# Kernel tuning notes

Measured on AMD Instinct MI355X. Metric: run time of the kernel, lower is better.

Reference implementation:

```python
import jax, jax.numpy as jnp
import numpy as np

N_NODES = 100000
N_EDGES = 1600000
D_IN, D_HID, D_OUT = 128, 128, 64


def _mean_agg(h_src_feat, src, dst, num_nodes):
    # gather source features along edges, scatter-sum into destinations,
    # divide by in-degree (clamped to 1, matching DGL zero-degree handling)
    summed = jax.ops.segment_sum(h_src_feat[src], dst, num_segments=num_nodes)
    deg = jax.ops.segment_sum(jnp.ones((src.shape[0],), h_src_feat.dtype), dst,
                              num_segments=num_nodes)
    return summed / jnp.maximum(deg, 1.0)[:, None]


def setup_inputs() -> dict:
    key = jax.random.key(0)
    ks = jax.random.split(key, 8)
    x = jax.random.normal(ks[0], (N_NODES, D_IN), dtype=jnp.float32)
    src = jax.random.randint(ks[1], (N_EDGES,), 0, N_NODES, dtype=jnp.int64)
    dst = jax.random.randint(ks[2], (N_EDGES,), 0, N_NODES, dtype=jnp.int64)
    s1 = 1.0 / np.sqrt(D_IN)
    s2 = 1.0 / np.sqrt(D_HID)
    W_self1 = jax.random.normal(ks[3], (D_IN, D_HID), dtype=jnp.float32) * s1
    W_neigh1 = jax.random.normal(ks[4], (D_IN, D_HID), dtype=jnp.float32) * s1
    b1 = jnp.zeros((D_HID,), dtype=jnp.float32)
    W_self2 = jax.random.normal(ks[5], (D_HID, D_OUT), dtype=jnp.float32) * s2
    W_neigh2 = jax.random.normal(ks[6], (D_HID, D_OUT), dtype=jnp.float32) * s2
    b2 = jnp.zeros((D_OUT,), dtype=jnp.float32)
    return {"x": x, "src": src, "dst": dst,
            "W_self1": W_self1, "W_neigh1": W_neigh1, "b1": b1,
            "W_self2": W_self2, "W_neigh2": W_neigh2, "b2": b2}


def reference(x, src, dst, W_self1, W_neigh1, b1, W_self2, W_neigh2, b2):
    n = x.shape[0]
    # layer 1: SAGEConv(mean) + ReLU (dropout is identity in eval mode)
    agg1 = _mean_agg(x, src, dst, n)
    h = x @ W_self1 + agg1 @ W_neigh1 + b1
    h = jax.nn.relu(h)
    # layer 2: SAGEConv(mean)
    agg2 = _mean_agg(h, src, dst, n)
    out = h @ W_self2 + agg2 @ W_neigh2 + b2
    return out
```

## Files before the change

kernel.cpp:

```cpp
#include <hip/hip_runtime.h>

#define N_NODES 100000
#define N_EDGES 1600000
#define D 128
#define D_OUT 64
#define MAXDEG 64

#define NBUCK 196
#define BCAP  12288
#define CHUNK 6400
#define NBLK_A (N_EDGES / CHUNK)
#define NBLK_CVT 6250
#define NBLK_PACK 24

typedef __attribute__((ext_vector_type(8))) short short8;
typedef __attribute__((ext_vector_type(4))) float floatx4;
typedef __attribute__((ext_vector_type(2))) float floatx2;

__device__ inline unsigned short f2bf(float f) {
    unsigned u = __builtin_bit_cast(unsigned, f);
    u = (u + 0x7fffu + ((u >> 16) & 1u)) >> 16;
    return (unsigned short)u;
}

__device__ inline void pack_dev(const float* __restrict__ Wa, const float* __restrict__ Wb,
                                int ncols, unsigned short* __restrict__ out, int t) {
    int nnt = ncols >> 4;
    int lane = t & 63;
    int nt = (t >> 6) % nnt;
    int kt = t / (64 * nnt);
    int col = nt * 16 + (lane & 15);
    int k0 = kt * 32 + ((lane >> 4) << 3);
    unsigned short* dstp = out + (size_t)((kt * nnt + nt) * 64 + lane) * 8;
    #pragma unroll
    for (int j = 0; j < 8; ++j) {
        int k = k0 + j;
        float f = (k < 128) ? Wa[(size_t)k * ncols + col]
                            : Wb[(size_t)(k - 128) * ncols + col];
        dstp[j] = f2bf(f);
    }
}

__global__ __launch_bounds__(256) void prep(
        const float* __restrict__ x, const int* __restrict__ src, const int* __restrict__ dst,
        const float* __restrict__ Ws1, const float* __restrict__ Wn1,
        const float* __restrict__ Ws2, const float* __restrict__ Wn2,
        unsigned short* __restrict__ xb, unsigned* __restrict__ xf8,
        int* __restrict__ gcur, int* __restrict__ bucketbuf,
        unsigned short* __restrict__ Wp1, unsigned short* __restrict__ Wp2) {
    __shared__ int cnt[NBUCK];
    __shared__ int base_s[NBUCK];
    const int tid = threadIdx.x;
    const int b = blockIdx.x;

    if (b < NBLK_A) {
        for (int i = tid; i < NBUCK; i += 256) cnt[i] = 0;
        __syncthreads();
        const int e0 = b * CHUNK;
        for (int i = tid; i < CHUNK; i += 256) {
            int d = __builtin_nontemporal_load(dst + e0 + i);
            atomicAdd(&cnt[d >> 9], 1);
        }
        __syncthreads();
        for (int i = tid; i < NBUCK; i += 256) {
            int c = cnt[i];
            base_s[i] = c ? atomicAdd(&gcur[i], c) : 0;
            cnt[i] = 0;
        }
        __syncthreads();
        for (int i = tid; i < CHUNK; i += 256) {
            int d = __builtin_nontemporal_load(dst + e0 + i);
            int s = __builtin_nontemporal_load(src + e0 + i);
            int bk = d >> 9;
            int p = base_s[bk] + atomicAdd(&cnt[bk], 1);
            if (p < BCAP)
                bucketbuf[bk * BCAP + p] = ((d & 511) << 17) | s;
        }
    } else if (b < NBLK_A + NBLK_CVT) {
        int i = (b - NBLK_A) * 256 + tid;
        const float4* p = (const float4*)x + 2 * (size_t)i;
        float4 a = p[0], c = p[1];
        uint4 u;
        u.x = (unsigned)f2bf(a.x) | ((unsigned)f2bf(a.y) << 16);
        u.y = (unsigned)f2bf(a.z) | ((unsigned)f2bf(a.w) << 16);
        u.z = (unsigned)f2bf(c.x) | ((unsigned)f2bf(c.y) << 16);
        u.w = (unsigned)f2bf(c.z) | ((unsigned)f2bf(c.w) << 16);
        ((uint4*)xb)[i] = u;
        int v0 = __builtin_amdgcn_cvt_pk_fp8_f32(a.x, a.y, 0, false);
        v0     = __builtin_amdgcn_cvt_pk_fp8_f32(a.z, a.w, v0, true);
        int v1 = __builtin_amdgcn_cvt_pk_fp8_f32(c.x, c.y, 0, false);
        v1     = __builtin_amdgcn_cvt_pk_fp8_f32(c.z, c.w, v1, true);
        uint2 w8; w8.x = (unsigned)v0; w8.y = (unsigned)v1;
        ((uint2*)xf8)[i] = w8;
    } else {
        int sub = b - (NBLK_A + NBLK_CVT);
        if (sub < 16) pack_dev(Ws1, Wn1, D, Wp1, sub * 256 + tid);
        else          pack_dev(Ws2, Wn2, D_OUT, Wp2, (sub - 16) * 256 + tid);
    }
}

__global__ __launch_bounds__(256) void bucket_csr(
        const int* __restrict__ gcur, const int* __restrict__ bucketbuf,
        int* __restrict__ dcount, int* __restrict__ csrp) {
    __shared__ int lcnt[512];
    const int tid = threadIdx.x, b = blockIdx.x;
    for (int i = tid; i < 512; i += 256) lcnt[i] = 0;
    __syncthreads();
    int m = gcur[b]; if (m > BCAP) m = BCAP;
    const int* __restrict__ buf = bucketbuf + b * BCAP;
    for (int i = tid; i < m; i += 256) {
        int v = buf[i];
        int dloc = v >> 17, s = v & 0x1FFFF;
        int slot = atomicAdd(&lcnt[dloc], 1);
        if (slot < MAXDEG)
            csrp[(((size_t)(b << 9) + dloc) << 6) + slot] = s;
    }
    __syncthreads();
    for (int i = tid; i < 512; i += 256) {
        int node = (b << 9) + i;
        if (node < N_NODES) {
            int c = lcnt[i];
            dcount[node] = (c > MAXDEG) ? MAXDEG : c;
        }
    }
}

__global__ __launch_bounds__(256) void agg_fp8(
        const unsigned char* __restrict__ feat, const int* __restrict__ csrp,
        const int* __restrict__ dcount, unsigned short* __restrict__ out) {
    int w = (blockIdx.x * 256 + threadIdx.x) >> 6;
    int lane = threadIdx.x & 63;
    if (w >= N_NODES) return;
    int dg = __builtin_amdgcn_readfirstlane(dcount[w]);
    const int half = lane >> 5;
    const int c4 = (lane & 31) << 2;
    int idxv = csrp[((size_t)w << 6) + lane];
    float a0 = 0.f, a1 = 0.f, a2 = 0.f, a3 = 0.f;
    int j = 0;
    for (; j + 8 <= dg; j += 8) {
        int s[4]; unsigned v[4];
        #pragma unroll
        for (int u = 0; u < 4; ++u) s[u] = __shfl(idxv, j + 2 * u + half);
        #pragma unroll
        for (int u = 0; u < 4; ++u)
            v[u] = *(const unsigned*)(feat + ((size_t)s[u] << 7) + c4);
        #pragma unroll
        for (int u = 0; u < 4; ++u) {
            floatx2 lo = __builtin_amdgcn_cvt_pk_f32_fp8(v[u], false);
            floatx2 hi = __builtin_amdgcn_cvt_pk_f32_fp8(v[u], true);
            a0 += lo.x; a1 += lo.y; a2 += hi.x; a3 += hi.y;
        }
    }
    for (; j + 2 <= dg; j += 2) {
        int s = __shfl(idxv, j + half);
        unsigned v = *(const unsigned*)(feat + ((size_t)s << 7) + c4);
        floatx2 lo = __builtin_amdgcn_cvt_pk_f32_fp8(v, false);
        floatx2 hi = __builtin_amdgcn_cvt_pk_f32_fp8(v, true);
        a0 += lo.x; a1 += lo.y; a2 += hi.x; a3 += hi.y;
    }
    if (j < dg) {
        int s = __shfl(idxv, j);
        if (half == 0) {
            unsigned v = *(const unsigned*)(feat + ((size_t)s << 7) + c4);
            floatx2 lo = __builtin_amdgcn_cvt_pk_f32_fp8(v, false);
            floatx2 hi = __builtin_amdgcn_cvt_pk_f32_fp8(v, true);
            a0 += lo.x; a1 += lo.y; a2 += hi.x; a3 += hi.y;
        }
    }
    a0 += __shfl_down(a0, 32); a1 += __shfl_down(a1, 32);
    a2 += __shfl_down(a2, 32); a3 += __shfl_down(a3, 32);
    if (half == 0) {
        float invd = (dg > 0) ? 1.0f / (float)dg : 1.0f;
        uint2 pv;
        pv.x = (unsigned)f2bf(a0 * invd) | ((unsigned)f2bf(a1 * invd) << 16);
        pv.y = (unsigned)f2bf(a2 * invd) | ((unsigned)f2bf(a3 * invd) << 16);
        *(uint2*)(out + (size_t)w * D + c4) = pv;
    }
}

template<int NT, bool RELU, bool OUT_BF16, bool WFP8>
__global__ __launch_bounds__(256) void gemm_sage(
        const unsigned short* __restrict__ A0, const unsigned short* __restrict__ A1,
        const unsigned short* __restrict__ Wp, const float* __restrict__ bias,
        void* __restrict__ Cout, unsigned char* __restrict__ C8)
{
    const int wave = threadIdx.x >> 6;
    const int lane = threadIdx.x & 63;
    const int q = lane >> 4, m = lane & 15;
    const int NCOL = NT * 16;

    int row = blockIdx.x * 64 + wave * 16 + m;
    int rowc = (row < N_NODES) ? row : (N_NODES - 1);

    floatx4 acc[NT];
    #pragma unroll
    for (int nt = 0; nt < NT; ++nt) acc[nt] = (floatx4){0.f, 0.f, 0.f, 0.f};

    #pragma unroll
    for (int kt = 0; kt < 8; ++kt) {
        const unsigned short* __restrict__ base = (kt < 4) ? A0 : A1;
        short8 af = *(const short8*)(base + (size_t)rowc * D + (kt & 3) * 32 + q * 8);
        #pragma unroll
        for (int nt = 0; nt < NT; ++nt) {
            short8 bf = *(const short8*)(Wp + (size_t)((kt * NT + nt) * 64 + lane) * 8);
            acc[nt] = __builtin_amdgcn_mfma_f32_16x16x32_bf16(af, bf, acc[nt], 0, 0, 0);
        }
    }

    const int orow_base = blockIdx.x * 64 + wave * 16 + q * 4;
    #pragma unroll
    for (int nt = 0; nt < NT; ++nt) {
        float b = bias[nt * 16 + m];
        #pragma unroll
        for (int i = 0; i < 4; ++i) {
            int orow = orow_base + i;
            if (orow < N_NODES) {
                float v = acc[nt][i] + b;
                if (RELU) v = fmaxf(v, 0.f);
                if (OUT_BF16)
                    ((unsigned short*)Cout)[(size_t)orow * NCOL + nt * 16 + m] = f2bf(v);
                else
                    ((float*)Cout)[(size_t)orow * NCOL + nt * 16 + m] = v;
                if (WFP8) {
                    int pk = __builtin_amdgcn_cvt_pk_fp8_f32(v, v, 0, false);
                    C8[(size_t)orow * NCOL + nt * 16 + m] = (unsigned char)(pk & 0xff);
                }
            }
        }
    }
}

extern "C" void kernel_launch(void* const* d_in, const int* in_sizes, int n_in,
                              void* d_out, int out_size, void* d_ws, size_t ws_size,
                              hipStream_t stream) {
    const float* x   = (const float*)d_in[0];
    const int*   src = (const int*)d_in[1];
    const int*   dst = (const int*)d_in[2];
    const float* Ws1 = (const float*)d_in[3];
    const float* Wn1 = (const float*)d_in[4];
    const float* b1  = (const float*)d_in[5];
    const float* Ws2 = (const float*)d_in[6];
    const float* Wn2 = (const float*)d_in[7];
    const float* b2  = (const float*)d_in[8];
    float* out = (float*)d_out;

    const size_t nd = (size_t)N_NODES * D;
    unsigned short* xb   = (unsigned short*)d_ws;
    unsigned short* h    = xb + nd;
    unsigned short* aggb = h + nd;
    unsigned char*  xf8  = (unsigned char*)(aggb + nd);
    unsigned char*  hf8  = xf8 + nd;
    int* dcount = (int*)(hf8 + nd);
    int* csrp   = dcount + N_NODES;
    int* gcur   = csrp + (size_t)N_NODES * MAXDEG;
    int* bucketbuf = gcur + 256;
    unsigned short* Wp1 = (unsigned short*)(bucketbuf + (size_t)NBUCK * BCAP);
    unsigned short* Wp2 = Wp1 + 32768;

    hipMemsetAsync(gcur, 0, NBUCK * sizeof(int), stream);

    prep<<<NBLK_A + NBLK_CVT + NBLK_PACK, 256, 0, stream>>>(
        x, src, dst, Ws1, Wn1, Ws2, Wn2, xb, (unsigned*)xf8, gcur, bucketbuf, Wp1, Wp2);
    bucket_csr<<<NBUCK, 256, 0, stream>>>(gcur, bucketbuf, dcount, csrp);

    const int agg_blocks = (N_NODES * 64 + 255) / 256;
    const int gemm_blocks = (N_NODES + 63) / 64;

    agg_fp8<<<agg_blocks, 256, 0, stream>>>(xf8, csrp, dcount, aggb);
    gemm_sage<8, true, true, true><<<gemm_blocks, 256, 0, stream>>>(xb, aggb, Wp1, b1, h, hf8);
    agg_fp8<<<agg_blocks, 256, 0, stream>>>(hf8, csrp, dcount, aggb);
    gemm_sage<4, false, false, false><<<gemm_blocks, 256, 0, stream>>>(h, aggb, Wp2, b2, out, nullptr);
}
```

Measured before the change: 305.4 us.

## Build padded CSR directly with global atomics, drop bucket pass

Replaces the two-pass bucketed CSR construction (LDS-counted bucketing into a staging buffer, then a separate per-bucket kernel) with a single pass in prep where each edge does a global atomicAdd on its destination's degree counter and writes its source into the padded slot. This removes one kernel launch and the staging-buffer write and read. In exchange it adds 1.6M scattered global atomics and scattered stores, and the degree counter is no longer clamped in place, so the aggregation kernel now clamps it to MAXDEG.

```diff
diff --git a/kernel.cpp b/kernel.cpp
--- a/kernel.cpp
+++ b/kernel.cpp
@@ -6,10 +6,7 @@
 #define D_OUT 64
 #define MAXDEG 64
 
-#define NBUCK 196
-#define BCAP  12288
-#define CHUNK 6400
-#define NBLK_A (N_EDGES / CHUNK)
+#define NBLK_CSR 1563
 #define NBLK_CVT 6250
 #define NBLK_PACK 24
 
@@ -46,38 +43,27 @@
         const float* __restrict__ Ws1, const float* __restrict__ Wn1,
         const float* __restrict__ Ws2, const float* __restrict__ Wn2,
         unsigned short* __restrict__ xb, unsigned* __restrict__ xf8,
-        int* __restrict__ gcur, int* __restrict__ bucketbuf,
+        int* __restrict__ dcount, int* __restrict__ csrp,
         unsigned short* __restrict__ Wp1, unsigned short* __restrict__ Wp2) {
-    __shared__ int cnt[NBUCK];
-    __shared__ int base_s[NBUCK];
     const int tid = threadIdx.x;
     const int b = blockIdx.x;
 
-    if (b < NBLK_A) {
-        for (int i = tid; i < NBUCK; i += 256) cnt[i] = 0;
-        __syncthreads();
-        const int e0 = b * CHUNK;
-        for (int i = tid; i < CHUNK; i += 256) {
-            int d = __builtin_nontemporal_load(dst + e0 + i);
-            atomicAdd(&cnt[d >> 9], 1);
-        }
-        __syncthreads();
-        for (int i = tid; i < NBUCK; i += 256) {
-            int c = cnt[i];
-            base_s[i] = c ? atomicAdd(&gcur[i], c) : 0;
-            cnt[i] = 0;
-        }
-        __syncthreads();
-        for (int i = tid; i < CHUNK; i += 256) {
-            int d = __builtin_nontemporal_load(dst + e0 + i);
-            int s = __builtin_nontemporal_load(src + e0 + i);
-            int bk = d >> 9;
-            int p = base_s[bk] + atomicAdd(&cnt[bk], 1);
-            if (p < BCAP)
-                bucketbuf[bk * BCAP + p] = ((d & 511) << 17) | s;
-        }
-    } else if (b < NBLK_A + NBLK_CVT) {
-        int i = (b - NBLK_A) * 256 + tid;
+    if (b < NBLK_CSR) {
+        int g = b * 256 + tid;
+        if (g < N_EDGES / 4) {
+            int4 d4 = ((const int4*)dst)[g];
+            int4 s4 = ((const int4*)src)[g];
+            int dd[4] = {d4.x, d4.y, d4.z, d4.w};
+            int ss[4] = {s4.x, s4.y, s4.z, s4.w};
+            #pragma unroll
+            for (int u = 0; u < 4; ++u) {
+                int p = atomicAdd(&dcount[dd[u]], 1);
+                if (p < MAXDEG)
+                    csrp[((size_t)dd[u] << 6) + p] = ss[u];
+            }
+        }
+    } else if (b < NBLK_CSR + NBLK_CVT) {
+        int i = (b - NBLK_CSR) * 256 + tid;
         const float4* p = (const float4*)x + 2 * (size_t)i;
         float4 a = p[0], c = p[1];
         uint4 u;
@@ -93,35 +79,9 @@
         uint2 w8; w8.x = (unsigned)v0; w8.y = (unsigned)v1;
         ((uint2*)xf8)[i] = w8;
     } else {
-        int sub = b - (NBLK_A + NBLK_CVT);
+        int sub = b - (NBLK_CSR + NBLK_CVT);
         if (sub < 16) pack_dev(Ws1, Wn1, D, Wp1, sub * 256 + tid);
         else          pack_dev(Ws2, Wn2, D_OUT, Wp2, (sub - 16) * 256 + tid);
-    }
-}
-
-__global__ __launch_bounds__(256) void bucket_csr(
-        const int* __restrict__ gcur, const int* __restrict__ bucketbuf,
-        int* __restrict__ dcount, int* __restrict__ csrp) {
-    __shared__ int lcnt[512];
-    const int tid = threadIdx.x, b = blockIdx.x;
-    for (int i = tid; i < 512; i += 256) lcnt[i] = 0;
-    __syncthreads();
-    int m = gcur[b]; if (m > BCAP) m = BCAP;
-    const int* __restrict__ buf = bucketbuf + b * BCAP;
-    for (int i = tid; i < m; i += 256) {
-        int v = buf[i];
-        int dloc = v >> 17, s = v & 0x1FFFF;
-        int slot = atomicAdd(&lcnt[dloc], 1);
-        if (slot < MAXDEG)
-            csrp[(((size_t)(b << 9) + dloc) << 6) + slot] = s;
-    }
-    __syncthreads();
-    for (int i = tid; i < 512; i += 256) {
-        int node = (b << 9) + i;
-        if (node < N_NODES) {
-            int c = lcnt[i];
-            dcount[node] = (c > MAXDEG) ? MAXDEG : c;
-        }
     }
 }
 
@@ -132,6 +92,7 @@
     int lane = threadIdx.x & 63;
     if (w >= N_NODES) return;
     int dg = __builtin_amdgcn_readfirstlane(dcount[w]);
+    if (dg > MAXDEG) dg = MAXDEG;
     const int half = lane >> 5;
     const int c4 = (lane & 31) << 2;
     int idxv = csrp[((size_t)w << 6) + lane];
@@ -252,16 +213,13 @@
     unsigned char*  hf8  = xf8 + nd;
     int* dcount = (int*)(hf8 + nd);
     int* csrp   = dcount + N_NODES;
-    int* gcur   = csrp + (size_t)N_NODES * MAXDEG;
-    int* bucketbuf = gcur + 256;
-    unsigned short* Wp1 = (unsigned short*)(bucketbuf + (size_t)NBUCK * BCAP);
+    unsigned short* Wp1 = (unsigned short*)(csrp + (size_t)N_NODES * MAXDEG);
     unsigned short* Wp2 = Wp1 + 32768;
 
-    hipMemsetAsync(gcur, 0, NBUCK * sizeof(int), stream);
-
-    prep<<<NBLK_A + NBLK_CVT + NBLK_PACK, 256, 0, stream>>>(
-        x, src, dst, Ws1, Wn1, Ws2, Wn2, xb, (unsigned*)xf8, gcur, bucketbuf, Wp1, Wp2);
-    bucket_csr<<<NBUCK, 256, 0, stream>>>(gcur, bucketbuf, dcount, csrp);
+    hipMemsetAsync(dcount, 0, N_NODES * sizeof(int), stream);
+
+    prep<<<NBLK_CSR + NBLK_CVT + NBLK_PACK, 256, 0, stream>>>(
+        x, src, dst, Ws1, Wn1, Ws2, Wn2, xb, (unsigned*)xf8, dcount, csrp, Wp1, Wp2);
 
     const int agg_blocks = (N_NODES * 64 + 255) / 256;
     const int gemm_blocks = (N_NODES + 63) / 64;
```

Result: slower. 392.5 us (+28.5%).

## Fuse neighbor aggregation into SAGE GEMM via LDS and shrink buckets

Applied to the files above, without the earlier changes.

Aggregation and the dense GEMM are merged into one kernel per layer. Each block aggregates its 64 destination rows into padded LDS as bf16 and then feeds them straight to MFMA, so the aggregated tensor no longer makes a global round-trip. The separate bf16 copy of x is dropped and x is converted from fp32 inside the GEMM. The CSR bucketing uses 782 smaller buckets of 128 nodes to spread the work across more blocks. In exchange, each fused block handles 64 nodes serially per wave (16 per wave), which lowers gather parallelism and latency hiding compared with one wave per node.

```diff
diff --git a/kernel.cpp b/kernel.cpp
--- a/kernel.cpp
+++ b/kernel.cpp
@@ -6,12 +6,15 @@
 #define D_OUT 64
 #define MAXDEG 64
 
-#define NBUCK 196
-#define BCAP  12288
+#define NBUCK 782
+#define BSHIFT 7
+#define BCAP  3072
 #define CHUNK 6400
 #define NBLK_A (N_EDGES / CHUNK)
 #define NBLK_CVT 6250
 #define NBLK_PACK 24
+
+#define LDSPAD 136
 
 typedef __attribute__((ext_vector_type(8))) short short8;
 typedef __attribute__((ext_vector_type(4))) float floatx4;
@@ -45,7 +48,7 @@
         const float* __restrict__ x, const int* __restrict__ src, const int* __restrict__ dst,
         const float* __restrict__ Ws1, const float* __restrict__ Wn1,
         const float* __restrict__ Ws2, const float* __restrict__ Wn2,
-        unsigned short* __restrict__ xb, unsigned* __restrict__ xf8,
+        unsigned* __restrict__ xf8,
         int* __restrict__ gcur, int* __restrict__ bucketbuf,
         unsigned short* __restrict__ Wp1, unsigned short* __restrict__ Wp2) {
     __shared__ int cnt[NBUCK];
@@ -59,7 +62,7 @@
         const int e0 = b * CHUNK;
         for (int i = tid; i < CHUNK; i += 256) {
             int d = __builtin_nontemporal_load(dst + e0 + i);
-            atomicAdd(&cnt[d >> 9], 1);
+            atomicAdd(&cnt[d >> BSHIFT], 1);
         }
         __syncthreads();
         for (int i = tid; i < NBUCK; i += 256) {
@@ -71,21 +74,15 @@
         for (int i = tid; i < CHUNK; i += 256) {
             int d = __builtin_nontemporal_load(dst + e0 + i);
             int s = __builtin_nontemporal_load(src + e0 + i);
-            int bk = d >> 9;
+            int bk = d >> BSHIFT;
             int p = base_s[bk] + atomicAdd(&cnt[bk], 1);
             if (p < BCAP)
-                bucketbuf[bk * BCAP + p] = ((d & 511) << 17) | s;
+                bucketbuf[bk * BCAP + p] = ((d & 127) << 17) | s;
         }
     } else if (b < NBLK_A + NBLK_CVT) {
         int i = (b - NBLK_A) * 256 + tid;
         const float4* p = (const float4*)x + 2 * (size_t)i;
         float4 a = p[0], c = p[1];
-        uint4 u;
-        u.x = (unsigned)f2bf(a.x) | ((unsigned)f2bf(a.y) << 16);
-        u.y = (unsigned)f2bf(a.z) | ((unsigned)f2bf(a.w) << 16);
-        u.z = (unsigned)f2bf(c.x) | ((unsigned)f2bf(c.y) << 16);
-        u.w = (unsigned)f2bf(c.z) | ((unsigned)f2bf(c.w) << 16);
-        ((uint4*)xb)[i] = u;
         int v0 = __builtin_amdgcn_cvt_pk_fp8_f32(a.x, a.y, 0, false);
         v0     = __builtin_amdgcn_cvt_pk_fp8_f32(a.z, a.w, v0, true);
         int v1 = __builtin_amdgcn_cvt_pk_fp8_f32(c.x, c.y, 0, false);
@@ -102,9 +99,9 @@
 __global__ __launch_bounds__(256) void bucket_csr(
         const int* __restrict__ gcur, const int* __restrict__ bucketbuf,
         int* __restrict__ dcount, int* __restrict__ csrp) {
-    __shared__ int lcnt[512];
+    __shared__ int lcnt[128];
     const int tid = threadIdx.x, b = blockIdx.x;
-    for (int i = tid; i < 512; i += 256) lcnt[i] = 0;
+    if (tid < 128) lcnt[tid] = 0;
     __syncthreads();
     int m = gcur[b]; if (m > BCAP) m = BCAP;
     const int* __restrict__ buf = bucketbuf + b * BCAP;
@@ -113,84 +110,87 @@
         int dloc = v >> 17, s = v & 0x1FFFF;
         int slot = atomicAdd(&lcnt[dloc], 1);
         if (slot < MAXDEG)
-            csrp[(((size_t)(b << 9) + dloc) << 6) + slot] = s;
+            csrp[(((size_t)(b << BSHIFT) + dloc) << 6) + slot] = s;
     }
     __syncthreads();
-    for (int i = tid; i < 512; i += 256) {
-        int node = (b << 9) + i;
+    if (tid < 128) {
+        int node = (b << BSHIFT) + tid;
         if (node < N_NODES) {
-            int c = lcnt[i];
+            int c = lcnt[tid];
             dcount[node] = (c > MAXDEG) ? MAXDEG : c;
         }
     }
 }
 
-__global__ __launch_bounds__(256) void agg_fp8(
+template<int NT, bool RELU, bool A0F32, bool OUT_BF16, bool WFP8>
+__global__ __launch_bounds__(256) void fused_sage(
+        const void* __restrict__ A0,
         const unsigned char* __restrict__ feat, const int* __restrict__ csrp,
-        const int* __restrict__ dcount, unsigned short* __restrict__ out) {
-    int w = (blockIdx.x * 256 + threadIdx.x) >> 6;
-    int lane = threadIdx.x & 63;
-    if (w >= N_NODES) return;
-    int dg = __builtin_amdgcn_readfirstlane(dcount[w]);
-    const int half = lane >> 5;
-    const int c4 = (lane & 31) << 2;
-    int idxv = csrp[((size_t)w << 6) + lane];
-    float a0 = 0.f, a1 = 0.f, a2 = 0.f, a3 = 0.f;
-    int j = 0;
-    for (; j + 8 <= dg; j += 8) {
-        int s[4]; unsigned v[4];
-        #pragma unroll
-        for (int u = 0; u < 4; ++u) s[u] = __shfl(idxv, j + 2 * u + half);
-        #pragma unroll
-        for (int u = 0; u < 4; ++u)
-            v[u] = *(const unsigned*)(feat + ((size_t)s[u] << 7) + c4);
-        #pragma unroll
-        for (int u = 0; u < 4; ++u) {
-            floatx2 lo = __builtin_amdgcn_cvt_pk_f32_fp8(v[u], false);
-            floatx2 hi = __builtin_amdgcn_cvt_pk_f32_fp8(v[u], true);
-            a0 += lo.x; a1 += lo.y; a2 += hi.x; a3 += hi.y;
-        }
-    }
-    for (; j + 2 <= dg; j += 2) {
-        int s = __shfl(idxv, j + half);
-        unsigned v = *(const unsigned*)(feat + ((size_t)s << 7) + c4);
-        floatx2 lo = __builtin_amdgcn_cvt_pk_f32_fp8(v, false);
-        floatx2 hi = __builtin_amdgcn_cvt_pk_f32_fp8(v, true);
-        a0 += lo.x; a1 += lo.y; a2 += hi.x; a3 += hi.y;
-    }
-    if (j < dg) {
-        int s = __shfl(idxv, j);
-        if (half == 0) {
-            unsigned v = *(const unsigned*)(feat + ((size_t)s << 7) + c4);
-            floatx2 lo = __builtin_amdgcn_cvt_pk_f32_fp8(v, false);
-            floatx2 hi = __builtin_amdgcn_cvt_pk_f32_fp8(v, true);
-            a0 += lo.x; a1 += lo.y; a2 += hi.x; a3 += hi.y;
-        }
-    }
-    a0 += __shfl_down(a0, 32); a1 += __shfl_down(a1, 32);
-    a2 += __shfl_down(a2, 32); a3 += __shfl_down(a3, 32);
-    if (half == 0) {
-        float invd = (dg > 0) ? 1.0f / (float)dg : 1.0f;
-        uint2 pv;
-        pv.x = (unsigned)f2bf(a0 * invd) | ((unsigned)f2bf(a1 * invd) << 16);
-        pv.y = (unsigned)f2bf(a2 * invd) | ((unsigned)f2bf(a3 * invd) << 16);
-        *(uint2*)(out + (size_t)w * D + c4) = pv;
-    }
-}
-
-template<int NT, bool RELU, bool OUT_BF16, bool WFP8>
-__global__ __launch_bounds__(256) void gemm_sage(
-        const unsigned short* __restrict__ A0, const unsigned short* __restrict__ A1,
+        const int* __restrict__ dcount,
         const unsigned short* __restrict__ Wp, const float* __restrict__ bias,
         void* __restrict__ Cout, unsigned char* __restrict__ C8)
 {
+    __shared__ unsigned short lds_agg[64 * LDSPAD];
     const int wave = threadIdx.x >> 6;
     const int lane = threadIdx.x & 63;
+    const int half = lane >> 5;
+    const int c4 = (lane & 31) << 2;
+
+    for (int t = 0; t < 16; ++t) {
+        const int n = blockIdx.x * 64 + wave * 16 + t;
+        float a0 = 0.f, a1 = 0.f, a2 = 0.f, a3 = 0.f;
+        int dg = 0;
+        if (n < N_NODES) {
+            dg = __builtin_amdgcn_readfirstlane(dcount[n]);
+            int idxv = csrp[((size_t)n << 6) + lane];
+            int j = 0;
+            for (; j + 8 <= dg; j += 8) {
+                int s[4]; unsigned v[4];
+                #pragma unroll
+                for (int u = 0; u < 4; ++u) s[u] = __shfl(idxv, j + 2 * u + half);
+                #pragma unroll
+                for (int u = 0; u < 4; ++u)
+                    v[u] = *(const unsigned*)(feat + ((size_t)s[u] << 7) + c4);
+                #pragma unroll
+                for (int u = 0; u < 4; ++u) {
+                    floatx2 lo = __builtin_amdgcn_cvt_pk_f32_fp8(v[u], false);
+                    floatx2 hi = __builtin_amdgcn_cvt_pk_f32_fp8(v[u], true);
+                    a0 += lo.x; a1 += lo.y; a2 += hi.x; a3 += hi.y;
+                }
+            }
+            for (; j + 2 <= dg; j += 2) {
+                int s = __shfl(idxv, j + half);
+                unsigned v = *(const unsigned*)(feat + ((size_t)s << 7) + c4);
+                floatx2 lo = __builtin_amdgcn_cvt_pk_f32_fp8(v, false);
+                floatx2 hi = __builtin_amdgcn_cvt_pk_f32_fp8(v, true);
+                a0 += lo.x; a1 += lo.y; a2 += hi.x; a3 += hi.y;
+            }
+            if (j < dg) {
+                int s = __shfl(idxv, j);
+                if (half == 0) {
+                    unsigned v = *(const unsigned*)(feat + ((size_t)s << 7) + c4);
+                    floatx2 lo = __builtin_amdgcn_cvt_pk_f32_fp8(v, false);
+                    floatx2 hi = __builtin_amdgcn_cvt_pk_f32_fp8(v, true);
+                    a0 += lo.x; a1 += lo.y; a2 += hi.x; a3 += hi.y;
+                }
+            }
+        }
+        a0 += __shfl_down(a0, 32); a1 += __shfl_down(a1, 32);
+        a2 += __shfl_down(a2, 32); a3 += __shfl_down(a3, 32);
+        if (half == 0) {
+            float invd = (dg > 0) ? 1.0f / (float)dg : 1.0f;
+            uint2 pv;
+            pv.x = (unsigned)f2bf(a0 * invd) | ((unsigned)f2bf(a1 * invd) << 16);
+            pv.y = (unsigned)f2bf(a2 * invd) | ((unsigned)f2bf(a3 * invd) << 16);
+            *(uint2*)(&lds_agg[(wave * 16 + t) * LDSPAD + c4]) = pv;
+        }
+    }
+    __syncthreads();
+
     const int q = lane >> 4, m = lane & 15;
     const int NCOL = NT * 16;
-
-    int row = blockIdx.x * 64 + wave * 16 + m;
-    int rowc = (row < N_NODES) ? row : (N_NODES - 1);
+    const int row = blockIdx.x * 64 + wave * 16 + m;
+    const int rowc = (row < N_NODES) ? row : (N_NODES - 1);
 
     floatx4 acc[NT];
     #pragma unroll
@@ -198,8 +198,24 @@
 
     #pragma unroll
     for (int kt = 0; kt < 8; ++kt) {
-        const unsigned short* __restrict__ base = (kt < 4) ? A0 : A1;
-        short8 af = *(const short8*)(base + (size_t)rowc * D + (kt & 3) * 32 + q * 8);
+        short8 af;
+        if (kt < 4) {
+            if (A0F32) {
+                const float* xr = (const float*)A0 + (size_t)rowc * D + kt * 32 + q * 8;
+                float4 f0 = *(const float4*)xr;
+                float4 f1 = *(const float4*)(xr + 4);
+                af[0] = (short)f2bf(f0.x); af[1] = (short)f2bf(f0.y);
+                af[2] = (short)f2bf(f0.z); af[3] = (short)f2bf(f0.w);
+                af[4] = (short)f2bf(f1.x); af[5] = (short)f2bf(f1.y);
+                af[6] = (short)f2bf(f1.z); af[7] = (short)f2bf(f1.w);
+            } else {
+                af = *(const short8*)((const unsigned short*)A0 +
+                                      (size_t)rowc * D + kt * 32 + q * 8);
+            }
+        } else {
+            af = *(const short8*)(&lds_agg[(wave * 16 + m) * LDSPAD +
+                                           (kt & 3) * 32 + q * 8]);
+        }
         #pragma unroll
         for (int nt = 0; nt < NT; ++nt) {
             short8 bf = *(const short8*)(Wp + (size_t)((kt * NT + nt) * 64 + lane) * 8);
@@ -210,12 +226,12 @@
     const int orow_base = blockIdx.x * 64 + wave * 16 + q * 4;
     #pragma unroll
     for (int nt = 0; nt < NT; ++nt) {
-        float b = bias[nt * 16 + m];
+        float bv = bias[nt * 16 + m];
         #pragma unroll
         for (int i = 0; i < 4; ++i) {
             int orow = orow_base + i;
             if (orow < N_NODES) {
-                float v = acc[nt][i] + b;
+                float v = acc[nt][i] + bv;
                 if (RELU) v = fmaxf(v, 0.f);
                 if (OUT_BF16)
                     ((unsigned short*)Cout)[(size_t)orow * NCOL + nt * 16 + m] = f2bf(v);
@@ -245,29 +261,25 @@
     float* out = (float*)d_out;
 
     const size_t nd = (size_t)N_NODES * D;
-    unsigned short* xb   = (unsigned short*)d_ws;
-    unsigned short* h    = xb + nd;
-    unsigned short* aggb = h + nd;
-    unsigned char*  xf8  = (unsigned char*)(aggb + nd);
-    unsigned char*  hf8  = xf8 + nd;
+    unsigned short* h   = (unsigned short*)d_ws;
+    unsigned char*  xf8 = (unsigned char*)(h + nd);
+    unsigned char*  hf8 = xf8 + nd;
     int* dcount = (int*)(hf8 + nd);
     int* csrp   = dcount + N_NODES;
     int* gcur   = csrp + (size_t)N_NODES * MAXDEG;
-    int* bucketbuf = gcur + 256;
+    int* bucketbuf = gcur + 1024;
     unsigned short* Wp1 = (unsigned short*)(bucketbuf + (size_t)NBUCK * BCAP);
     unsigned short* Wp2 = Wp1 + 32768;
 
     hipMemsetAsync(gcur, 0, NBUCK * sizeof(int), stream);
 
     prep<<<NBLK_A + NBLK_CVT + NBLK_PACK, 256, 0, stream>>>(
-        x, src, dst, Ws1, Wn1, Ws2, Wn2, xb, (unsigned*)xf8, gcur, bucketbuf, Wp1, Wp2);
+        x, src, dst, Ws1, Wn1, Ws2, Wn2, (unsigned*)xf8, gcur, bucketbuf, Wp1, Wp2);
     bucket_csr<<<NBUCK, 256, 0, stream>>>(gcur, bucketbuf, dcount, csrp);
 
-    const int agg_blocks = (N_NODES * 64 + 255) / 256;
-    const int gemm_blocks = (N_NODES + 63) / 64;
-
-    agg_fp8<<<agg_blocks, 256, 0, stream>>>(xf8, csrp, dcount, aggb);
-    gemm_sage<8, true, true, true><<<gemm_blocks, 256, 0, stream>>>(xb, aggb, Wp1, b1, h, hf8);
-    agg_fp8<<<agg_blocks, 256, 0, stream>>>(hf8, csrp, dcount, aggb);
-    gemm_sage<4, false, false, false><<<gemm_blocks, 256, 0, stream>>>(h, aggb, Wp2, b2, out, nullptr);
-}
+    const int fused_blocks = (N_NODES + 63) / 64;
+    fused_sage<8, true,  true,  true,  true ><<<fused_blocks, 256, 0, stream>>>(
+        x, xf8, csrp, dcount, Wp1, b1, h, hf8);
+    fused_sage<4, false, false, false, false><<<fused_blocks, 256, 0, stream>>>(
+        h, hf8, csrp, dcount, Wp2, b2, out, nullptr);
+}
```

Result: slower. 347.1 us (+13.7%).

## Transform before aggregating and split edge bucketing into finer buckets

Applied to the files above, without the earlier changes.

The layer maths is reordered so each GEMM runs first on node features, producing the self term and an fp8 neighbour-projected term. Aggregation then gathers the projected rows and adds them to the self term, with ReLU fused into the layer-1 aggregation. Layer 2 therefore gathers 64-wide rows instead of 128-wide ones, and each GEMM drops to K=128. Edge bucketing now runs as its own kernel with finer buckets (128 nodes each) and caches dst in LDS, while CSR building is fused into the feature-conversion kernel. The cost is that rounding neighbour contributions to fp8 after the projection can change accuracy.

```diff
diff --git a/kernel.cpp b/kernel.cpp
--- a/kernel.cpp
+++ b/kernel.cpp
@@ -6,10 +6,12 @@
 #define D_OUT 64
 #define MAXDEG 64
 
-#define NBUCK 196
-#define BCAP  12288
-#define CHUNK 6400
-#define NBLK_A (N_EDGES / CHUNK)
+#define NBUCK 782
+#define BSHIFT 7
+#define BCAP  3072
+#define NBLK_SPLIT 500
+#define CHUNK 3200
+#define NBLK_CSR NBUCK
 #define NBLK_CVT 6250
 #define NBLK_PACK 24
 
@@ -22,62 +24,95 @@
     u = (u + 0x7fffu + ((u >> 16) & 1u)) >> 16;
     return (unsigned short)u;
 }
-
-__device__ inline void pack_dev(const float* __restrict__ Wa, const float* __restrict__ Wb,
-                                int ncols, unsigned short* __restrict__ out, int t) {
-    int nnt = ncols >> 4;
+__device__ inline float bf2f(unsigned short u) {
+    return __builtin_bit_cast(float, (unsigned)u << 16);
+}
+
+__device__ inline void pack_ncat(const float* __restrict__ Wa, const float* __restrict__ Wb,
+                                 int ncA, int ncB, unsigned short* __restrict__ out, int t) {
+    int nnt = (ncA + ncB) >> 4;
     int lane = t & 63;
     int nt = (t >> 6) % nnt;
     int kt = t / (64 * nnt);
     int col = nt * 16 + (lane & 15);
     int k0 = kt * 32 + ((lane >> 4) << 3);
+    const float* W = (col < ncA) ? Wa : Wb;
+    int nc = (col < ncA) ? ncA : ncB;
+    int c  = (col < ncA) ? col : col - ncA;
     unsigned short* dstp = out + (size_t)((kt * nnt + nt) * 64 + lane) * 8;
     #pragma unroll
-    for (int j = 0; j < 8; ++j) {
-        int k = k0 + j;
-        float f = (k < 128) ? Wa[(size_t)k * ncols + col]
-                            : Wb[(size_t)(k - 128) * ncols + col];
-        dstp[j] = f2bf(f);
-    }
-}
-
-__global__ __launch_bounds__(256) void prep(
-        const float* __restrict__ x, const int* __restrict__ src, const int* __restrict__ dst,
+    for (int j = 0; j < 8; ++j)
+        dstp[j] = f2bf(W[(size_t)(k0 + j) * nc + c]);
+}
+
+__global__ __launch_bounds__(256) void split_k(
+        const int* __restrict__ src, const int* __restrict__ dst,
+        int* __restrict__ gcur, int* __restrict__ bucketbuf) {
+    __shared__ int cnt[NBUCK];
+    __shared__ int base_s[NBUCK];
+    __shared__ int dstc[CHUNK];
+    const int tid = threadIdx.x;
+    const int e0 = blockIdx.x * CHUNK;
+    for (int i = tid; i < NBUCK; i += 256) cnt[i] = 0;
+    __syncthreads();
+    for (int i = tid; i < CHUNK; i += 256) {
+        int d = __builtin_nontemporal_load(dst + e0 + i);
+        dstc[i] = d;
+        atomicAdd(&cnt[d >> BSHIFT], 1);
+    }
+    __syncthreads();
+    for (int i = tid; i < NBUCK; i += 256) {
+        int c = cnt[i];
+        base_s[i] = c ? atomicAdd(&gcur[i], c) : 0;
+        cnt[i] = 0;
+    }
+    __syncthreads();
+    for (int i = tid; i < CHUNK; i += 256) {
+        int d = dstc[i];
+        int s = __builtin_nontemporal_load(src + e0 + i);
+        int bk = d >> BSHIFT;
+        int p = base_s[bk] + atomicAdd(&cnt[bk], 1);
+        if (p < BCAP)
+            bucketbuf[bk * BCAP + p] = ((d & 127) << 17) | s;
+    }
+}
+
+__global__ __launch_bounds__(256) void prep2(
+        const float* __restrict__ x,
+        const int* __restrict__ gcur, const int* __restrict__ bucketbuf,
         const float* __restrict__ Ws1, const float* __restrict__ Wn1,
         const float* __restrict__ Ws2, const float* __restrict__ Wn2,
-        unsigned short* __restrict__ xb, unsigned* __restrict__ xf8,
-        int* __restrict__ gcur, int* __restrict__ bucketbuf,
+        unsigned short* __restrict__ xb,
+        int* __restrict__ dcount, int* __restrict__ csrp,
         unsigned short* __restrict__ Wp1, unsigned short* __restrict__ Wp2) {
-    __shared__ int cnt[NBUCK];
-    __shared__ int base_s[NBUCK];
-    const int tid = threadIdx.x;
-    const int b = blockIdx.x;
-
-    if (b < NBLK_A) {
-        for (int i = tid; i < NBUCK; i += 256) cnt[i] = 0;
+    const int tid = threadIdx.x, b = blockIdx.x;
+    if (b < NBLK_CSR) {
+        __shared__ int lcnt[128];
+        if (tid < 128) lcnt[tid] = 0;
         __syncthreads();
-        const int e0 = b * CHUNK;
-        for (int i = tid; i < CHUNK; i += 256) {
-            int d = __builtin_nontemporal_load(dst + e0 + i);
-            atomicAdd(&cnt[d >> 9], 1);
+        int m = gcur[b]; if (m > BCAP) m = BCAP;
+        const int* __restrict__ buf = bucketbuf + b * BCAP;
+        for (int i = tid; i < m; i += 256) {
+            int v = buf[i];
+            int dloc = (v >> 17) & 127, s = v & 0x1FFFF;
+            int node = (b << BSHIFT) + dloc;
+            int slot = atomicAdd(&lcnt[dloc], 1);
+            if (slot < MAXDEG && node < N_NODES)
+                csrp[((size_t)node << 6) + slot] = s;
         }
         __syncthreads();
-        for (int i = tid; i < NBUCK; i += 256) {
-            int c = cnt[i];
-            base_s[i] = c ? atomicAdd(&gcur[i], c) : 0;
-            cnt[i] = 0;
-        }
-        __syncthreads();
-        for (int i = tid; i < CHUNK; i += 256) {
-            int d = __builtin_nontemporal_load(dst + e0 + i);
-            int s = __builtin_nontemporal_load(src + e0 + i);
-            int bk = d >> 9;
-            int p = base_s[bk] + atomicAdd(&cnt[bk], 1);
-            if (p < BCAP)
-                bucketbuf[bk * BCAP + p] = ((d & 511) << 17) | s;
-        }
-    } else if (b < NBLK_A + NBLK_CVT) {
-        int i = (b - NBLK_A) * 256 + tid;
+        if (tid < 128) {
+            int node = (b << BSHIFT) + tid;
+            if (node < N_NODES) {
+                int c = lcnt[tid]; if (c > MAXDEG) c = MAXDEG;
+                dcount[node] = c;
+                int cf = (c + 15) & ~15; if (cf > MAXDEG) cf = MAXDEG;
+                int* row = csrp + ((size_t)node << 6);
+                for (int k = c; k < cf; ++k) row[k] = 0;
+            }
+        }
+    } else if (b < NBLK_CSR + NBLK_CVT) {
+        int i = (b - NBLK_CSR) * 256 + tid;
         const float4* p = (const float4*)x + 2 * (size_t)i;
         float4 a = p[0], c = p[1];
         uint4 u;
@@ -86,146 +121,140 @@
         u.z = (unsigned)f2bf(c.x) | ((unsigned)f2bf(c.y) << 16);
         u.w = (unsigned)f2bf(c.z) | ((unsigned)f2bf(c.w) << 16);
         ((uint4*)xb)[i] = u;
-        int v0 = __builtin_amdgcn_cvt_pk_fp8_f32(a.x, a.y, 0, false);
-        v0     = __builtin_amdgcn_cvt_pk_fp8_f32(a.z, a.w, v0, true);
-        int v1 = __builtin_amdgcn_cvt_pk_fp8_f32(c.x, c.y, 0, false);
-        v1     = __builtin_amdgcn_cvt_pk_fp8_f32(c.z, c.w, v1, true);
-        uint2 w8; w8.x = (unsigned)v0; w8.y = (unsigned)v1;
-        ((uint2*)xf8)[i] = w8;
     } else {
-        int sub = b - (NBLK_A + NBLK_CVT);
-        if (sub < 16) pack_dev(Ws1, Wn1, D, Wp1, sub * 256 + tid);
-        else          pack_dev(Ws2, Wn2, D_OUT, Wp2, (sub - 16) * 256 + tid);
-    }
-}
-
-__global__ __launch_bounds__(256) void bucket_csr(
-        const int* __restrict__ gcur, const int* __restrict__ bucketbuf,
-        int* __restrict__ dcount, int* __restrict__ csrp) {
-    __shared__ int lcnt[512];
-    const int tid = threadIdx.x, b = blockIdx.x;
-    for (int i = tid; i < 512; i += 256) lcnt[i] = 0;
-    __syncthreads();
-    int m = gcur[b]; if (m > BCAP) m = BCAP;
-    const int* __restrict__ buf = bucketbuf + b * BCAP;
-    for (int i = tid; i < m; i += 256) {
-        int v = buf[i];
-        int dloc = v >> 17, s = v & 0x1FFFF;
-        int slot = atomicAdd(&lcnt[dloc], 1);
-        if (slot < MAXDEG)
-            csrp[(((size_t)(b << 9) + dloc) << 6) + slot] = s;
-    }
-    __syncthreads();
-    for (int i = tid; i < 512; i += 256) {
-        int node = (b << 9) + i;
-        if (node < N_NODES) {
-            int c = lcnt[i];
-            dcount[node] = (c > MAXDEG) ? MAXDEG : c;
-        }
-    }
-}
-
-__global__ __launch_bounds__(256) void agg_fp8(
+        int sub = b - (NBLK_CSR + NBLK_CVT);
+        if (sub < 16) pack_ncat(Ws1, Wn1, D, D, Wp1, sub * 256 + tid);
+        else          pack_ncat(Ws2, Wn2, D_OUT, D_OUT, Wp2, (sub - 16) * 256 + tid);
+    }
+}
+
+template<int NTA, int NTB, bool OUTA_BF16>
+__global__ __launch_bounds__(256) void gemm_dual(
+        const unsigned short* __restrict__ A, const unsigned short* __restrict__ Wp,
+        const float* __restrict__ bias, void* __restrict__ OutA,
+        unsigned char* __restrict__ OutB)
+{
+    const int NT = NTA + NTB;
+    const int wave = threadIdx.x >> 6;
+    const int lane = threadIdx.x & 63;
+    const int q = lane >> 4, m = lane & 15;
+
+    int row = blockIdx.x * 64 + wave * 16 + m;
+    int rowc = (row < N_NODES) ? row : (N_NODES - 1);
+
+    floatx4 acc[NT];
+    #pragma unroll
+    for (int nt = 0; nt < NT; ++nt) acc[nt] = (floatx4){0.f, 0.f, 0.f, 0.f};
+
+    #pragma unroll
+    for (int kt = 0; kt < 4; ++kt) {
+        short8 af = *(const short8*)(A + (size_t)rowc * D + kt * 32 + q * 8);
+        #pragma unroll
+        for (int nt = 0; nt < NT; ++nt) {
+            short8 bf = *(const short8*)(Wp + (size_t)((kt * NT + nt) * 64 + lane) * 8);
+            acc[nt] = __builtin_amdgcn_mfma_f32_16x16x32_bf16(af, bf, acc[nt], 0, 0, 0);
+        }
+    }
+
+    const int orow_base = blockIdx.x * 64 + wave * 16 + q * 4;
+    #pragma unroll
+    for (int nt = 0; nt < NT; ++nt) {
+        float bv = (nt < NTA) ? bias[nt * 16 + m] : 0.f;
+        #pragma unroll
+        for (int i = 0; i < 4; ++i) {
+            int orow = orow_base + i;
+            if (orow < N_NODES) {
+                float v = acc[nt][i];
+                if (nt < NTA) {
+                    v += bv;
+                    if (OUTA_BF16)
+                        ((unsigned short*)OutA)[(size_t)orow * (NTA * 16) + nt * 16 + m] = f2bf(v);
+                    else
+                        ((float*)OutA)[(size_t)orow * (NTA * 16) + nt * 16 + m] = v;
+                } else {
+                    int pk = __builtin_amdgcn_cvt_pk_fp8_f32(v, v, 0, false);
+                    OutB[(size_t)orow * (NTB * 16) + (nt - NTA) * 16 + m] =
+                        (unsigned char)(pk & 0xff);
+                }
+            }
+        }
+    }
+}
+
+template<bool L1>
+__global__ __launch_bounds__(256) void agg_add(
         const unsigned char* __restrict__ feat, const int* __restrict__ csrp,
-        const int* __restrict__ dcount, unsigned short* __restrict__ out) {
+        const int* __restrict__ dcount, const void* __restrict__ self,
+        void* __restrict__ out)
+{
+    const int EPG = L1 ? 4 : 8;
+    const int LPE = 64 / EPG;
+    const int FSH = L1 ? 7 : 6;
+    const int NC  = L1 ? 128 : 64;
+
     int w = (blockIdx.x * 256 + threadIdx.x) >> 6;
     int lane = threadIdx.x & 63;
     if (w >= N_NODES) return;
     int dg = __builtin_amdgcn_readfirstlane(dcount[w]);
-    const int half = lane >> 5;
-    const int c4 = (lane & 31) << 2;
+    const int g = lane / LPE;
+    const int l = lane % LPE;
     int idxv = csrp[((size_t)w << 6) + lane];
+
     float a0 = 0.f, a1 = 0.f, a2 = 0.f, a3 = 0.f;
-    int j = 0;
-    for (; j + 8 <= dg; j += 8) {
-        int s[4]; unsigned v[4];
+    float a4 = 0.f, a5 = 0.f, a6 = 0.f, a7 = 0.f;
+    for (int j = 0; j < dg; j += 16) {
         #pragma unroll
-        for (int u = 0; u < 4; ++u) s[u] = __shfl(idxv, j + 2 * u + half);
-        #pragma unroll
-        for (int u = 0; u < 4; ++u)
-            v[u] = *(const unsigned*)(feat + ((size_t)s[u] << 7) + c4);
-        #pragma unroll
-        for (int u = 0; u < 4; ++u) {
-            floatx2 lo = __builtin_amdgcn_cvt_pk_f32_fp8(v[u], false);
-            floatx2 hi = __builtin_amdgcn_cvt_pk_f32_fp8(v[u], true);
-            a0 += lo.x; a1 += lo.y; a2 += hi.x; a3 += hi.y;
-        }
-    }
-    for (; j + 2 <= dg; j += 2) {
-        int s = __shfl(idxv, j + half);
-        unsigned v = *(const unsigned*)(feat + ((size_t)s << 7) + c4);
-        floatx2 lo = __builtin_amdgcn_cvt_pk_f32_fp8(v, false);
-        floatx2 hi = __builtin_amdgcn_cvt_pk_f32_fp8(v, true);
-        a0 += lo.x; a1 += lo.y; a2 += hi.x; a3 += hi.y;
-    }
-    if (j < dg) {
-        int s = __shfl(idxv, j);
-        if (half == 0) {
-            unsigned v = *(const unsigned*)(feat + ((size_t)s << 7) + c4);
-            floatx2 lo = __builtin_amdgcn_cvt_pk_f32_fp8(v, false);
-            floatx2 hi = __builtin_amdgcn_cvt_pk_f32_fp8(v, true);
-            a0 += lo.x; a1 += lo.y; a2 += hi.x; a3 += hi.y;
-        }
-    }
-    a0 += __shfl_down(a0, 32); a1 += __shfl_down(a1, 32);
-    a2 += __shfl_down(a2, 32); a3 += __shfl_down(a3, 32);
-    if (half == 0) {
+        for (int u = 0; u < 16 / EPG; ++u) {
+            int e = j + u * EPG + g;
+            int s = __shfl(idxv, e);
+            uint2 v = *(const uint2*)(feat + ((size_t)s << FSH) + (l << 3));
+            bool ok = e < dg;
+            unsigned vx = ok ? v.x : 0u;
+            unsigned vy = ok ? v.y : 0u;
+            floatx2 f0 = __builtin_amdgcn_cvt_pk_f32_fp8(vx, false);
+            floatx2 f1 = __builtin_amdgcn_cvt_pk_f32_fp8(vx, true);
+            floatx2 f2 = __builtin_amdgcn_cvt_pk_f32_fp8(vy, false);
+            floatx2 f3 = __builtin_amdgcn_cvt_pk_f32_fp8(vy, true);
+            a0 += f0.x; a1 += f0.y; a2 += f1.x; a3 += f1.y;
+            a4 += f2.x; a5 += f2.y; a6 += f3.x; a7 += f3.y;
+        }
+    }
+    #pragma unroll
+    for (int step = 0; step < 3; ++step) {
+        int delta = 32 >> step;
+        if (delta >= LPE) {
+            a0 += __shfl_down(a0, delta); a1 += __shfl_down(a1, delta);
+            a2 += __shfl_down(a2, delta); a3 += __shfl_down(a3, delta);
+            a4 += __shfl_down(a4, delta); a5 += __shfl_down(a5, delta);
+            a6 += __shfl_down(a6, delta); a7 += __shfl_down(a7, delta);
+        }
+    }
+    if (g == 0) {
         float invd = (dg > 0) ? 1.0f / (float)dg : 1.0f;
-        uint2 pv;
-        pv.x = (unsigned)f2bf(a0 * invd) | ((unsigned)f2bf(a1 * invd) << 16);
-        pv.y = (unsigned)f2bf(a2 * invd) | ((unsigned)f2bf(a3 * invd) << 16);
-        *(uint2*)(out + (size_t)w * D + c4) = pv;
-    }
-}
-
-template<int NT, bool RELU, bool OUT_BF16, bool WFP8>
-__global__ __launch_bounds__(256) void gemm_sage(
-        const unsigned short* __restrict__ A0, const unsigned short* __restrict__ A1,
-        const unsigned short* __restrict__ Wp, const float* __restrict__ bias,
-        void* __restrict__ Cout, unsigned char* __restrict__ C8)
-{
-    const int wave = threadIdx.x >> 6;
-    const int lane = threadIdx.x & 63;
-    const int q = lane >> 4, m = lane & 15;
-    const int NCOL = NT * 16;
-
-    int row = blockIdx.x * 64 + wave * 16 + m;
-    int rowc = (row < N_NODES) ? row : (N_NODES - 1);
-
-    floatx4 acc[NT];
-    #pragma unroll
-    for (int nt = 0; nt < NT; ++nt) acc[nt] = (floatx4){0.f, 0.f, 0.f, 0.f};
-
-    #pragma unroll
-    for (int kt = 0; kt < 8; ++kt) {
-        const unsigned short* __restrict__ base = (kt < 4) ? A0 : A1;
-        short8 af = *(const short8*)(base + (size_t)rowc * D + (kt & 3) * 32 + q * 8);
-        #pragma unroll
-        for (int nt = 0; nt < NT; ++nt) {
-            short8 bf = *(const short8*)(Wp + (size_t)((kt * NT + nt) * 64 + lane) * 8);
-            acc[nt] = __builtin_amdgcn_mfma_f32_16x16x32_bf16(af, bf, acc[nt], 0, 0, 0);
-        }
-    }
-
-    const int orow_base = blockIdx.x * 64 + wave * 16 + q * 4;
-    #pragma unroll
-    for (int nt = 0; nt < NT; ++nt) {
-        float b = bias[nt * 16 + m];
-        #pragma unroll
-        for (int i = 0; i < 4; ++i) {
-            int orow = orow_base + i;
-            if (orow < N_NODES) {
-                float v = acc[nt][i] + b;
-                if (RELU) v = fmaxf(v, 0.f);
-                if (OUT_BF16)
-                    ((unsigned short*)Cout)[(size_t)orow * NCOL + nt * 16 + m] = f2bf(v);
-                else
-                    ((float*)Cout)[(size_t)orow * NCOL + nt * 16 + m] = v;
-                if (WFP8) {
-                    int pk = __builtin_amdgcn_cvt_pk_fp8_f32(v, v, 0, false);
-                    C8[(size_t)orow * NCOL + nt * 16 + m] = (unsigned char)(pk & 0xff);
-                }
+        if (L1) {
+            const unsigned short* sp = (const unsigned short*)self + (size_t)w * NC + l * 8;
+            short8 sv = *(const short8*)sp;
+            short8 hv;
+            float acc[8] = {a0,a1,a2,a3,a4,a5,a6,a7};
+            #pragma unroll
+            for (int c = 0; c < 8; ++c) {
+                float hval = bf2f((unsigned short)sv[c]) + acc[c] * invd;
+                hval = fmaxf(hval, 0.f);
+                hv[c] = (short)f2bf(hval);
             }
+            *(short8*)((unsigned short*)out + (size_t)w * NC + l * 8) = hv;
+        } else {
+            const float* sp = (const float*)self + (size_t)w * NC + l * 8;
+            float4 s0 = *(const float4*)sp;
+            float4 s1 = *(const float4*)(sp + 4);
+            float4 o0, o1;
+            o0.x = s0.x + a0 * invd; o0.y = s0.y + a1 * invd;
+            o0.z = s0.z + a2 * invd; o0.w = s0.w + a3 * invd;
+            o1.x = s1.x + a4 * invd; o1.y = s1.y + a5 * invd;
+            o1.z = s1.z + a6 * invd; o1.w = s1.w + a7 * invd;
+            float* op = (float*)out + (size_t)w * NC + l * 8;
+            *(float4*)op = o0;
+            *(float4*)(op + 4) = o1;
         }
     }
 }
@@ -245,29 +274,30 @@
     float* out = (float*)d_out;
 
     const size_t nd = (size_t)N_NODES * D;
-    unsigned short* xb   = (unsigned short*)d_ws;
-    unsigned short* h    = xb + nd;
-    unsigned short* aggb = h + nd;
-    unsigned char*  xf8  = (unsigned char*)(aggb + nd);
-    unsigned char*  hf8  = xf8 + nd;
-    int* dcount = (int*)(hf8 + nd);
+    unsigned short* xb  = (unsigned short*)d_ws;
+    unsigned short* h   = xb;
+    unsigned short* xs  = xb + nd;
+    float*          tmp = (float*)xs;
+    unsigned char*  y8  = (unsigned char*)(xs + nd);
+    unsigned char*  z8  = y8;
+    int* dcount = (int*)(y8 + nd);
     int* csrp   = dcount + N_NODES;
     int* gcur   = csrp + (size_t)N_NODES * MAXDEG;
-    int* bucketbuf = gcur + 256;
+    int* bucketbuf = gcur + 1024;
     unsigned short* Wp1 = (unsigned short*)(bucketbuf + (size_t)NBUCK * BCAP);
     unsigned short* Wp2 = Wp1 + 32768;
 
     hipMemsetAsync(gcur, 0, NBUCK * sizeof(int), stream);
 
-    prep<<<NBLK_A + NBLK_CVT + NBLK_PACK, 256, 0, stream>>>(
-        x, src, dst, Ws1, Wn1, Ws2, Wn2, xb, (unsigned*)xf8, gcur, bucketbuf, Wp1, Wp2);
-    bucket_csr<<<NBUCK, 256, 0, stream>>>(gcur, bucketbuf, dcount, csrp);
-
-    const int agg_blocks = (N_NODES * 64 + 255) / 256;
+    split_k<<<NBLK_SPLIT, 256, 0, stream>>>(src, dst, gcur, bucketbuf);
+    prep2<<<NBLK_CSR + NBLK_CVT + NBLK_PACK, 256, 0, stream>>>(
+        x, gcur, bucketbuf, Ws1, Wn1, Ws2, Wn2, xb, dcount, csrp, Wp1, Wp2);
+
     const int gemm_blocks = (N_NODES + 63) / 64;
-
-    agg_fp8<<<agg_blocks, 256, 0, stream>>>(xf8, csrp, dcount, aggb);
-    gemm_sage<8, true, true, true><<<gemm_blocks, 256, 0, stream>>>(xb, aggb, Wp1, b1, h, hf8);
-    agg_fp8<<<agg_blocks, 256, 0, stream>>>(hf8, csrp, dcount, aggb);
-    gemm_sage<4, false, false, false><<<gemm_blocks, 256, 0, stream>>>(h, aggb, Wp2, b2, out, nullptr);
-}
+    const int agg_blocks  = (N_NODES * 64 + 255) / 256;
+
+    gemm_dual<8, 8, true ><<<gemm_blocks, 256, 0, stream>>>(xb, Wp1, b1, xs, y8);
+    agg_add<true ><<<agg_blocks, 256, 0, stream>>>(y8, csrp, dcount, xs, h);
+    gemm_dual<4, 4, false><<<gemm_blocks, 256, 0, stream>>>(h, Wp2, b2, tmp, z8);
+    agg_add<false><<<agg_blocks, 256, 0, stream>>>(z8, csrp, dcount, tmp, out);
+}
```

Result: slower. 320.0 us (+4.8%).
